# Optimization experiments

Measured on AMD Instinct MI355X. Metric: run time of the kernel, lower is better.

The kernel has to match this reference:

```python
import jax, jax.numpy as jnp
import numpy as np

N_EMBD = 2048
N_HEAD = 32
N_KV_HEADS = 8
HEAD_DIM = 64
N_REP = N_HEAD // N_KV_HEADS
MAX_SEQ_LEN = 4096
ROPE_THETA = 10000.0


def _precompute_freqs_cis(dim, end, theta=ROPE_THETA):
    freqs = 1.0 / theta ** (jnp.arange(0, dim, 2)[: dim // 2].astype(jnp.float32) / dim)
    t = jnp.arange(end, dtype=jnp.float32)
    freqs = jnp.outer(t, freqs)  # (end, dim//2)
    return jnp.cos(freqs), jnp.sin(freqs)


def setup_inputs() -> dict:
    key = jax.random.key(0)
    ks = jax.random.split(key, 5)
    B, S = 2, 2048
    x = jax.random.normal(ks[0], (B, S, N_EMBD), dtype=jnp.float32)
    # torch Linear(in, out, bias=False): y = x @ W.T, W is (out, in). We store (in, out).
    sc = 1.0 / np.sqrt(N_EMBD)
    wq = jax.random.normal(ks[1], (N_EMBD, N_EMBD), dtype=jnp.float32) * sc
    wk = jax.random.normal(ks[2], (N_EMBD, N_KV_HEADS * HEAD_DIM), dtype=jnp.float32) * sc
    wv = jax.random.normal(ks[3], (N_EMBD, N_KV_HEADS * HEAD_DIM), dtype=jnp.float32) * sc
    wo = jax.random.normal(ks[4], (N_EMBD, N_EMBD), dtype=jnp.float32) * sc
    freqs_cos, freqs_sin = _precompute_freqs_cis(HEAD_DIM, MAX_SEQ_LEN)
    return {"x": x, "wq": wq, "wk": wk, "wv": wv, "wo": wo,
            "freqs_cos": freqs_cos, "freqs_sin": freqs_sin}


def _apply_rotary(t, cos, sin):
    # t: (B, S, H, HD); interleaved real/imag pairs along last dim.
    shp = t.shape
    t2 = t.reshape(*shp[:-1], HEAD_DIM // 2, 2)
    r, i = t2[..., 0], t2[..., 1]
    out_r = r * cos - i * sin
    out_i = r * sin + i * cos
    return jnp.stack([out_r, out_i], axis=-1).reshape(shp)


def reference(x, wq, wk, wv, wo, freqs_cos, freqs_sin):
    B, S, _ = x.shape
    xq = (x @ wq).reshape(B, S, N_HEAD, HEAD_DIM)
    xk = (x @ wk).reshape(B, S, N_KV_HEADS, HEAD_DIM)
    xv = (x @ wv).reshape(B, S, N_KV_HEADS, HEAD_DIM)

    cos = freqs_cos[:S][None, :, None, :]  # (1, S, 1, HD/2)
    sin = freqs_sin[:S][None, :, None, :]
    xq = _apply_rotary(xq, cos, sin)
    xk = _apply_rotary(xk, cos, sin)

    # GQA: repeat KV heads (repeat_interleave along head dim)
    keys = jnp.repeat(xk, N_REP, axis=2)    # (B, S, H, HD)
    values = jnp.repeat(xv, N_REP, axis=2)

    scores = jnp.einsum('bqhd,bkhd->bhqk', xq, keys) / np.sqrt(HEAD_DIM)
    causal = jnp.tril(jnp.ones((S, S), dtype=bool))
    scores = jnp.where(causal, scores, -jnp.inf)
    probs = jax.nn.softmax(scores.astype(jnp.float32), axis=-1).astype(xq.dtype)
    out = jnp.einsum('bhqk,bkhd->bqhd', probs, values)  # (B, S, H, HD)
    out = out.reshape(B, S, N_EMBD)
    return out @ wo
```

## Files before the change

kernel.cpp:

```cpp
#include <hip/hip_runtime.h>
#include <hip/hip_fp16.h>
#include <stdint.h>

typedef _Float16 f16x8 __attribute__((ext_vector_type(8)));
typedef _Float16 f16x2 __attribute__((ext_vector_type(2)));
typedef float f32x4 __attribute__((ext_vector_type(4)));
typedef float f32x16 __attribute__((ext_vector_type(16)));

#define B_ 2
#define S_ 2048
#define NE 2048
#define NH 32
#define NKV 8
#define HD 64
#define NTOK (B_ * S_)
#define QKVN 3072

__device__ __forceinline__ void gld_lds16(void* lds, const void* g) {
  __builtin_amdgcn_global_load_lds(
      (const __attribute__((address_space(1))) void*)g,
      (__attribute__((address_space(3))) void*)lds, 16, 0, 0);
}

__global__ void conv_x_kernel(const float* __restrict__ x,
                              _Float16* __restrict__ xo, int n2) {
  int i = blockIdx.x * 256 + threadIdx.x;
  if (i < n2) {
    float2 v = ((const float2*)x)[i];
    f16x2 h;
    h.x = (_Float16)v.x;
    h.y = (_Float16)v.y;
    ((f16x2*)xo)[i] = h;
  }
}

__global__ void tconv_kernel(const float* __restrict__ src,
                             _Float16* __restrict__ dst,
                             int srcN, int rowoff, int ldd) {
  __shared__ float tile[32][33];
  int n0 = blockIdx.x * 32, k0 = blockIdx.y * 32;
  int tx = threadIdx.x, ty = threadIdx.y;
  for (int i = ty; i < 32; i += 8)
    tile[i][tx] = src[(size_t)(k0 + i) * srcN + n0 + tx];
  __syncthreads();
  for (int i = ty; i < 32; i += 8)
    dst[(size_t)(rowoff + n0 + i) * ldd + k0 + tx] = (_Float16)tile[tx][i];
}

template <int OUT_F32>
__global__ __launch_bounds__(256, 2) void gemm_bt(
    const _Float16* __restrict__ A, const _Float16* __restrict__ Bt,
    void* __restrict__ Cout, int M, int N, int K) {
  __shared__ _Float16 As[128 * 32];
  __shared__ _Float16 Bs[128 * 32];
  const int tid = threadIdx.x;
  const int wave = tid >> 6, lane = tid & 63;
  const int qd = lane >> 4, ln = lane & 15;
  const int m0 = blockIdx.y * 128, n0 = blockIdx.x * 128;
  const int wm = (wave >> 1) * 64, wn = (wave & 1) * 64;

  f32x4 acc[4][4] = {};

  const int srow = (lane >> 2);
  const int scol = (lane & 3) * 8;

  for (int k0 = 0; k0 < K; k0 += 32) {
    __syncthreads();
#pragma unroll
    for (int it = 0; it < 2; ++it) {
      int r = wave * 32 + it * 16 + srow;
      gld_lds16(&As[(wave * 32 + it * 16) * 32],
                A + (size_t)(m0 + r) * K + k0 + scol);
      gld_lds16(&Bs[(wave * 32 + it * 16) * 32],
                Bt + (size_t)(n0 + r) * K + k0 + scol);
    }
    __syncthreads();
    f16x8 a[4], b[4];
#pragma unroll
    for (int mt = 0; mt < 4; ++mt)
      a[mt] = *(const f16x8*)&As[(wm + mt * 16 + ln) * 32 + qd * 8];
#pragma unroll
    for (int nt = 0; nt < 4; ++nt)
      b[nt] = *(const f16x8*)&Bs[(wn + nt * 16 + ln) * 32 + qd * 8];
#pragma unroll
    for (int mt = 0; mt < 4; ++mt)
#pragma unroll
      for (int nt = 0; nt < 4; ++nt)
        acc[mt][nt] =
            __builtin_amdgcn_mfma_f32_16x16x32_f16(a[mt], b[nt], acc[mt][nt], 0, 0, 0);
  }

#pragma unroll
  for (int mt = 0; mt < 4; ++mt) {
    int row = m0 + wm + mt * 16 + qd * 4;
#pragma unroll
    for (int nt = 0; nt < 4; ++nt) {
      int col = n0 + wn + nt * 16 + ln;
#pragma unroll
      for (int r = 0; r < 4; ++r) {
        if (OUT_F32)
          ((float*)Cout)[(size_t)(row + r) * N + col] = acc[mt][nt][r];
        else
          ((_Float16*)Cout)[(size_t)(row + r) * N + col] =
              (_Float16)acc[mt][nt][r];
      }
    }
  }
}

__global__ void rope_scatter_kernel(const _Float16* __restrict__ qkv,
                                    const float* __restrict__ fcos,
                                    const float* __restrict__ fsin,
                                    _Float16* __restrict__ Qb,
                                    _Float16* __restrict__ Kb) {
  const float QSC = 0.125f * 1.44269504088896f;
  int idx = blockIdx.x * 256 + threadIdx.x;
  int t = idx / 1280;
  int col = (idx - t * 1280) * 2;
  int b = t >> 11, s = t & 2047;
  float v0 = (float)qkv[(size_t)t * QKVN + col];
  float v1 = (float)qkv[(size_t)t * QKVN + col + 1];
  _Float16* dst;
  size_t off;
  int d;
  float sc;
  if (col < 2048) {
    int h = col >> 6;
    d = col & 63;
    dst = Qb;
    off = ((size_t)(b * NH + h) * S_ + s) * HD + d;
    sc = QSC;
  } else {
    int cc = col - 2048;
    int h = cc >> 6;
    d = cc & 63;
    dst = Kb;
    off = ((size_t)(b * NKV + h) * S_ + s) * HD + d;
    sc = 1.0f;
  }
  float c = fcos[s * 32 + (d >> 1)], sn = fsin[s * 32 + (d >> 1)];
  f16x2 o;
  o.x = (_Float16)((v0 * c - v1 * sn) * sc);
  o.y = (_Float16)((v0 * sn + v1 * c) * sc);
  *(f16x2*)(dst + off) = o;
}

__global__ void vtrans_kernel(const _Float16* __restrict__ qkv,
                              _Float16* __restrict__ Vtg) {
  __shared__ _Float16 tile[64][65];
  int t0 = blockIdx.x * 64;
  int kv = blockIdx.y, b = blockIdx.z;
  int tid = threadIdx.x;
  for (int slot = tid; slot < 4096; slot += 256) {
    int r = slot >> 6, c = slot & 63;
    tile[r][c] = qkv[(size_t)(b * S_ + t0 + r) * QKVN + 2560 + kv * 64 + c];
  }
  __syncthreads();
  size_t base = ((size_t)(b * NKV + kv) * HD) * S_;
  for (int slot = tid; slot < 4096; slot += 256) {
    int d = slot >> 6, r = slot & 63;
    Vtg[base + (size_t)d * S_ + t0 + r] = tile[r][d];
  }
}

__global__ __launch_bounds__(256, 2) void attn_kernel(
    const _Float16* __restrict__ Qb, const _Float16* __restrict__ Kb,
    const _Float16* __restrict__ Vtg, _Float16* __restrict__ Ob) {
  constexpr int LDP = 72;
  constexpr float M_SHIFT = 10.0f;
  __shared__ _Float16 Ks[64 * 64];
  __shared__ _Float16 Vs[64 * 64];
  __shared__ _Float16 Ps[4 * 32 * LDP];
  const int tid = threadIdx.x;
  const int wave = tid >> 6, lane = tid & 63;
  const int mrow = lane & 31, half = lane >> 5;
  const int h = blockIdx.y, b = blockIdx.z;
  const int kvh = h >> 2;

  const _Float16* Qh = Qb + ((size_t)(b * NH + h) * S_) * HD;
  const _Float16* Kh = Kb + ((size_t)(b * NKV + kvh) * S_) * HD;
  const _Float16* Vh = Vtg + ((size_t)(b * NKV + kvh) * HD) * S_;

  const int sr = tid >> 3;
  const int scc = tid & 7;
  _Float16* Pw = &Ps[wave * 32 * LDP];

#pragma unroll
  for (int pass = 0; pass < 2; ++pass) {
    const int qt = pass ? blockIdx.x : (15 - blockIdx.x);
    const int q0 = qt * 128;
    const int nkt = 2 * qt + 2;

    const int qrow = q0 + wave * 32 + mrow;
    f16x8 aq[4];
#pragma unroll
    for (int kk = 0; kk < 4; ++kk)
      aq[kk] = *(const f16x8*)(Qh + (size_t)qrow * HD + kk * 16 + half * 8);

    f32x16 accO[2] = {};
    float lsum[16] = {};

    f16x8 kp[2], vp[2];
#pragma unroll
    for (int i = 0; i < 2; ++i) {
      kp[i] = *(const f16x8*)(Kh + (size_t)(i * 32 + sr) * HD + scc * 8);
      vp[i] = *(const f16x8*)(Vh + (size_t)(i * 32 + sr) * S_ + scc * 8);
    }
#pragma unroll
    for (int i = 0; i < 2; ++i) {
      int r = i * 32 + sr;
      *(f16x8*)&Ks[r * 64 + ((scc ^ (r & 7)) * 8)] = kp[i];
      *(f16x8*)&Vs[r * 64 + ((scc ^ (r & 7)) * 8)] = vp[i];
    }

    for (int kt = 0; kt < nkt; ++kt) {
      __syncthreads();
      if (kt + 1 < nkt) {
#pragma unroll
        for (int i = 0; i < 2; ++i) {
          kp[i] = *(const f16x8*)(Kh +
                                  (size_t)((kt + 1) * 64 + i * 32 + sr) * HD +
                                  scc * 8);
          vp[i] = *(const f16x8*)(Vh + (size_t)(i * 32 + sr) * S_ +
                                  (kt + 1) * 64 + scc * 8);
        }
      }

      f32x16 s[2];
#pragma unroll
      for (int nt = 0; nt < 2; ++nt)
#pragma unroll
        for (int r = 0; r < 16; ++r) s[nt][r] = -M_SHIFT;
#pragma unroll
      for (int kk = 0; kk < 4; ++kk) {
        int c = kk * 2 + half;
#pragma unroll
        for (int nt = 0; nt < 2; ++nt) {
          int key = nt * 32 + mrow;
          f16x8 bk = *(const f16x8*)&Ks[key * 64 + ((c ^ (key & 7)) * 8)];
          s[nt] = __builtin_amdgcn_mfma_f32_32x32x16_f16(aq[kk], bk, s[nt],
                                                         0, 0, 0);
        }
      }

      const bool edge = (kt >= nkt - 2);
#pragma unroll
      for (int nt = 0; nt < 2; ++nt)
#pragma unroll
        for (int r = 0; r < 16; ++r) {
          int rr = (r & 3) + 8 * (r >> 2) + 4 * half;
          float p = exp2f(s[nt][r]);
          if (edge) {
            int key = kt * 64 + nt * 32 + mrow;
            int qr = q0 + wave * 32 + rr;
            if (key > qr) p = 0.f;
          }
          lsum[r] += p;
          Pw[rr * LDP + nt * 32 + mrow] = (_Float16)p;
        }

      asm volatile("s_waitcnt lgkmcnt(0)" ::: "memory");
      f16x8 ap[4];
#pragma unroll
      for (int kk = 0; kk < 4; ++kk)
        ap[kk] = *(const f16x8*)&Pw[mrow * LDP + kk * 16 + half * 8];

#pragma unroll
      for (int kk = 0; kk < 4; ++kk) {
        int c = kk * 2 + half;
#pragma unroll
        for (int nt = 0; nt < 2; ++nt) {
          int d = nt * 32 + mrow;
          f16x8 bv = *(const f16x8*)&Vs[d * 64 + ((c ^ (d & 7)) * 8)];
          accO[nt] = __builtin_amdgcn_mfma_f32_32x32x16_f16(ap[kk], bv,
                                                            accO[nt], 0, 0, 0);
        }
      }

      __syncthreads();
      if (kt + 1 < nkt) {
#pragma unroll
        for (int i = 0; i < 2; ++i) {
          int r = i * 32 + sr;
          *(f16x8*)&Ks[r * 64 + ((scc ^ (r & 7)) * 8)] = kp[i];
          *(f16x8*)&Vs[r * 64 + ((scc ^ (r & 7)) * 8)] = vp[i];
        }
      }
    }

#pragma unroll
    for (int r = 0; r < 16; ++r) {
      float t = lsum[r];
#pragma unroll
      for (int off = 1; off <= 16; off <<= 1) t += __shfl_xor(t, off);
      float inv = 1.f / t;
      int rr = (r & 3) + 8 * (r >> 2) + 4 * half;
      int srow = q0 + wave * 32 + rr;
      size_t base = ((size_t)(b * S_) + srow) * NE + h * HD;
#pragma unroll
      for (int nt = 0; nt < 2; ++nt)
        Ob[base + nt * 32 + mrow] = (_Float16)(accO[nt][r] * inv);
    }
  }
}

extern "C" void kernel_launch(void* const* d_in, const int* in_sizes, int n_in,
                              void* d_out, int out_size, void* d_ws,
                              size_t ws_size, hipStream_t stream) {
  const float* x = (const float*)d_in[0];
  const float* wq = (const float*)d_in[1];
  const float* wk = (const float*)d_in[2];
  const float* wv = (const float*)d_in[3];
  const float* wo = (const float*)d_in[4];
  const float* fcos = (const float*)d_in[5];
  const float* fsin = (const float*)d_in[6];

  char* ws = (char*)d_ws;
  _Float16* xb = (_Float16*)(ws);
  _Float16* wqkv_t = (_Float16*)(ws + 16777216);
  _Float16* wo_t = (_Float16*)(ws + 29360128);
  _Float16* qkv = (_Float16*)(ws + 37748736);
  _Float16* Qb = (_Float16*)(ws + 62914560);
  _Float16* Kb = (_Float16*)(ws + 79691776);
  _Float16* Vb = (_Float16*)(ws + 83886080);
  _Float16* Ob = (_Float16*)(ws + 88080384);

  conv_x_kernel<<<16384, 256, 0, stream>>>(x, xb, (NTOK * NE) / 2);

  dim3 tb(32, 8);
  tconv_kernel<<<dim3(64, 64), tb, 0, stream>>>(wq, wqkv_t, 2048, 0, 2048);
  tconv_kernel<<<dim3(16, 64), tb, 0, stream>>>(wk, wqkv_t, 512, 2048, 2048);
  tconv_kernel<<<dim3(16, 64), tb, 0, stream>>>(wv, wqkv_t, 512, 2560, 2048);
  tconv_kernel<<<dim3(64, 64), tb, 0, stream>>>(wo, wo_t, 2048, 0, 2048);

  gemm_bt<0><<<dim3(QKVN / 128, NTOK / 128), 256, 0, stream>>>(
      xb, wqkv_t, qkv, NTOK, QKVN, NE);

  rope_scatter_kernel<<<(NTOK * 1280) / 256, 256, 0, stream>>>(qkv, fcos, fsin,
                                                               Qb, Kb);
  vtrans_kernel<<<dim3(S_ / 64, NKV, B_), 256, 0, stream>>>(qkv, Vb);

  attn_kernel<<<dim3(8, NH, B_), 256, 0, stream>>>(Qb, Kb, Vb, Ob);

  gemm_bt<1><<<dim3(NE / 128, NTOK / 128), 256, 0, stream>>>(
      Ob, wo_t, d_out, NTOK, NE, NE);
}
```

Before: 346.2 us.

## Keep attention P in registers via transposed MFMA and shrink query tile

The attention kernel swaps the MFMA operand order so scores come out transposed (keys by query). The probability tile can then be packed to fp16 and exchanged across wave halves with lane shuffles, replacing the round trip through shared memory. The query tile drops from 128 to 64 rows with 2 waves per block and twice the grid, row sums collapse to one scalar per lane, and output stores become packed 4-wide. This removes LDS traffic and a wait, at the cost of extra shuffles and less K/V reuse per block load.

```diff
diff --git a/kernel.cpp b/kernel.cpp
--- a/kernel.cpp
+++ b/kernel.cpp
@@ -3,6 +3,7 @@
 #include <stdint.h>
 
 typedef _Float16 f16x8 __attribute__((ext_vector_type(8)));
+typedef _Float16 f16x4 __attribute__((ext_vector_type(4)));
 typedef _Float16 f16x2 __attribute__((ext_vector_type(2)));
 typedef float f32x4 __attribute__((ext_vector_type(4)));
 typedef float f32x16 __attribute__((ext_vector_type(16)));
@@ -15,6 +16,10 @@
 #define HD 64
 #define NTOK (B_ * S_)
 #define QKVN 3072
+
+__device__ __forceinline__ f16x2 pk(float a, float b) {
+  return __builtin_bit_cast(f16x2, __builtin_amdgcn_cvt_pkrtz(a, b));
+}
 
 __device__ __forceinline__ void gld_lds16(void* lds, const void* g) {
   __builtin_amdgcn_global_load_lds(
@@ -163,17 +168,16 @@
   }
 }
 
-__global__ __launch_bounds__(256, 2) void attn_kernel(
+__global__ __launch_bounds__(128, 2) void attn_kernel(
     const _Float16* __restrict__ Qb, const _Float16* __restrict__ Kb,
     const _Float16* __restrict__ Vtg, _Float16* __restrict__ Ob) {
-  constexpr int LDP = 72;
   constexpr float M_SHIFT = 10.0f;
   __shared__ _Float16 Ks[64 * 64];
   __shared__ _Float16 Vs[64 * 64];
-  __shared__ _Float16 Ps[4 * 32 * LDP];
   const int tid = threadIdx.x;
   const int wave = tid >> 6, lane = tid & 63;
-  const int mrow = lane & 31, half = lane >> 5;
+  const int mrow = lane & 31;
+  const bool half = (lane >> 5) != 0;
   const int h = blockIdx.y, b = blockIdx.z;
   const int kvh = h >> 2;
 
@@ -183,45 +187,45 @@
 
   const int sr = tid >> 3;
   const int scc = tid & 7;
-  _Float16* Pw = &Ps[wave * 32 * LDP];
+  const int swz = (scc ^ (sr & 7)) * 8;
 
 #pragma unroll
   for (int pass = 0; pass < 2; ++pass) {
-    const int qt = pass ? blockIdx.x : (15 - blockIdx.x);
-    const int q0 = qt * 128;
-    const int nkt = 2 * qt + 2;
+    const int qt = pass ? blockIdx.x : (31 - blockIdx.x);
+    const int q0 = qt * 64;
+    const int nkt = qt + 1;
 
     const int qrow = q0 + wave * 32 + mrow;
     f16x8 aq[4];
 #pragma unroll
     for (int kk = 0; kk < 4; ++kk)
-      aq[kk] = *(const f16x8*)(Qh + (size_t)qrow * HD + kk * 16 + half * 8);
+      aq[kk] = *(const f16x8*)(Qh + (size_t)qrow * HD + kk * 16 +
+                               (half ? 8 : 0));
 
     f32x16 accO[2] = {};
-    float lsum[16] = {};
-
-    f16x8 kp[2], vp[2];
-#pragma unroll
-    for (int i = 0; i < 2; ++i) {
-      kp[i] = *(const f16x8*)(Kh + (size_t)(i * 32 + sr) * HD + scc * 8);
-      vp[i] = *(const f16x8*)(Vh + (size_t)(i * 32 + sr) * S_ + scc * 8);
-    }
-#pragma unroll
-    for (int i = 0; i < 2; ++i) {
-      int r = i * 32 + sr;
-      *(f16x8*)&Ks[r * 64 + ((scc ^ (r & 7)) * 8)] = kp[i];
-      *(f16x8*)&Vs[r * 64 + ((scc ^ (r & 7)) * 8)] = vp[i];
+    float lsum = 0.f;
+
+    f16x8 kp[4], vp[4];
+#pragma unroll
+    for (int i = 0; i < 4; ++i) {
+      kp[i] = *(const f16x8*)(Kh + (size_t)(sr + i * 16) * HD + scc * 8);
+      vp[i] = *(const f16x8*)(Vh + (size_t)(sr + i * 16) * S_ + scc * 8);
+    }
+#pragma unroll
+    for (int i = 0; i < 4; ++i) {
+      *(f16x8*)&Ks[(sr + i * 16) * 64 + swz] = kp[i];
+      *(f16x8*)&Vs[(sr + i * 16) * 64 + swz] = vp[i];
     }
 
     for (int kt = 0; kt < nkt; ++kt) {
       __syncthreads();
       if (kt + 1 < nkt) {
 #pragma unroll
-        for (int i = 0; i < 2; ++i) {
+        for (int i = 0; i < 4; ++i) {
           kp[i] = *(const f16x8*)(Kh +
-                                  (size_t)((kt + 1) * 64 + i * 32 + sr) * HD +
+                                  (size_t)((kt + 1) * 64 + sr + i * 16) * HD +
                                   scc * 8);
-          vp[i] = *(const f16x8*)(Vh + (size_t)(i * 32 + sr) * S_ +
+          vp[i] = *(const f16x8*)(Vh + (size_t)(sr + i * 16) * S_ +
                                   (kt + 1) * 64 + scc * 8);
         }
       }
@@ -233,74 +237,95 @@
         for (int r = 0; r < 16; ++r) s[nt][r] = -M_SHIFT;
 #pragma unroll
       for (int kk = 0; kk < 4; ++kk) {
-        int c = kk * 2 + half;
+        int c = kk * 2 + (half ? 1 : 0);
 #pragma unroll
         for (int nt = 0; nt < 2; ++nt) {
-          int key = nt * 32 + mrow;
-          f16x8 bk = *(const f16x8*)&Ks[key * 64 + ((c ^ (key & 7)) * 8)];
-          s[nt] = __builtin_amdgcn_mfma_f32_32x32x16_f16(aq[kk], bk, s[nt],
+          int krow = nt * 32 + mrow;
+          f16x8 bk = *(const f16x8*)&Ks[krow * 64 + ((c ^ (krow & 7)) * 8)];
+          s[nt] = __builtin_amdgcn_mfma_f32_32x32x16_f16(bk, aq[kk], s[nt],
                                                          0, 0, 0);
         }
       }
 
-      const bool edge = (kt >= nkt - 2);
+      const bool edge = (kt == nkt - 1);
+      float pf[2][16];
 #pragma unroll
       for (int nt = 0; nt < 2; ++nt)
 #pragma unroll
         for (int r = 0; r < 16; ++r) {
-          int rr = (r & 3) + 8 * (r >> 2) + 4 * half;
+          int key = kt * 64 + nt * 32 + (r & 3) + 8 * (r >> 2) +
+                    (half ? 4 : 0);
           float p = exp2f(s[nt][r]);
-          if (edge) {
-            int key = kt * 64 + nt * 32 + mrow;
-            int qr = q0 + wave * 32 + rr;
-            if (key > qr) p = 0.f;
-          }
-          lsum[r] += p;
-          Pw[rr * LDP + nt * 32 + mrow] = (_Float16)p;
-        }
-
-      asm volatile("s_waitcnt lgkmcnt(0)" ::: "memory");
-      f16x8 ap[4];
-#pragma unroll
-      for (int kk = 0; kk < 4; ++kk)
-        ap[kk] = *(const f16x8*)&Pw[mrow * LDP + kk * 16 + half * 8];
-
-#pragma unroll
-      for (int kk = 0; kk < 4; ++kk) {
-        int c = kk * 2 + half;
-#pragma unroll
-        for (int nt = 0; nt < 2; ++nt) {
-          int d = nt * 32 + mrow;
-          f16x8 bv = *(const f16x8*)&Vs[d * 64 + ((c ^ (d & 7)) * 8)];
-          accO[nt] = __builtin_amdgcn_mfma_f32_32x32x16_f16(ap[kk], bv,
-                                                            accO[nt], 0, 0, 0);
+          if (edge && key > qrow) p = 0.f;
+          lsum += p;
+          pf[nt][r] = p;
+        }
+
+      f16x2 P2[2][4][2];
+#pragma unroll
+      for (int nt = 0; nt < 2; ++nt)
+#pragma unroll
+        for (int c = 0; c < 4; ++c)
+#pragma unroll
+          for (int u = 0; u < 2; ++u)
+            P2[nt][c][u] = pk(pf[nt][4 * c + 2 * u], pf[nt][4 * c + 2 * u + 1]);
+
+#pragma unroll
+      for (int s4 = 0; s4 < 4; ++s4) {
+        const int ntp = s4 >> 1;
+        const int gA = (2 * s4) & 3, gB = (2 * s4 + 1) & 3;
+        f16x2 own0 = half ? P2[ntp][gB][0] : P2[ntp][gA][0];
+        f16x2 own1 = half ? P2[ntp][gB][1] : P2[ntp][gA][1];
+        f16x2 snd0 = half ? P2[ntp][gA][0] : P2[ntp][gB][0];
+        f16x2 snd1 = half ? P2[ntp][gA][1] : P2[ntp][gB][1];
+        f16x2 rcv0 = __builtin_bit_cast(
+            f16x2, __shfl_xor(__builtin_bit_cast(int, snd0), 32));
+        f16x2 rcv1 = __builtin_bit_cast(
+            f16x2, __shfl_xor(__builtin_bit_cast(int, snd1), 32));
+        union {
+          f16x2 h2[4];
+          f16x8 h8;
+        } bp;
+        bp.h2[0] = half ? rcv0 : own0;
+        bp.h2[1] = half ? rcv1 : own1;
+        bp.h2[2] = half ? own0 : rcv0;
+        bp.h2[3] = half ? own1 : rcv1;
+        const int c = 2 * s4 + (half ? 1 : 0);
+#pragma unroll
+        for (int ntd = 0; ntd < 2; ++ntd) {
+          int drow = ntd * 32 + mrow;
+          f16x8 bv = *(const f16x8*)&Vs[drow * 64 + ((c ^ (drow & 7)) * 8)];
+          accO[ntd] = __builtin_amdgcn_mfma_f32_32x32x16_f16(bv, bp.h8,
+                                                             accO[ntd], 0, 0, 0);
         }
       }
 
       __syncthreads();
       if (kt + 1 < nkt) {
 #pragma unroll
-        for (int i = 0; i < 2; ++i) {
-          int r = i * 32 + sr;
-          *(f16x8*)&Ks[r * 64 + ((scc ^ (r & 7)) * 8)] = kp[i];
-          *(f16x8*)&Vs[r * 64 + ((scc ^ (r & 7)) * 8)] = vp[i];
-        }
-      }
-    }
-
-#pragma unroll
-    for (int r = 0; r < 16; ++r) {
-      float t = lsum[r];
-#pragma unroll
-      for (int off = 1; off <= 16; off <<= 1) t += __shfl_xor(t, off);
-      float inv = 1.f / t;
-      int rr = (r & 3) + 8 * (r >> 2) + 4 * half;
-      int srow = q0 + wave * 32 + rr;
-      size_t base = ((size_t)(b * S_) + srow) * NE + h * HD;
-#pragma unroll
-      for (int nt = 0; nt < 2; ++nt)
-        Ob[base + nt * 32 + mrow] = (_Float16)(accO[nt][r] * inv);
-    }
+        for (int i = 0; i < 4; ++i) {
+          *(f16x8*)&Ks[(sr + i * 16) * 64 + swz] = kp[i];
+          *(f16x8*)&Vs[(sr + i * 16) * 64 + swz] = vp[i];
+        }
+      }
+    }
+
+    float tot = lsum + __shfl_xor(lsum, 32);
+    float inv = 1.f / tot;
+    size_t base = ((size_t)(b * S_) + qrow) * NE + h * HD;
+#pragma unroll
+    for (int ntd = 0; ntd < 2; ++ntd)
+#pragma unroll
+      for (int rq = 0; rq < 4; ++rq) {
+        int d0 = ntd * 32 + 8 * rq + (half ? 4 : 0);
+        union {
+          f16x2 h2[2];
+          f16x4 h4;
+        } o;
+        o.h2[0] = pk(accO[ntd][4 * rq + 0] * inv, accO[ntd][4 * rq + 1] * inv);
+        o.h2[1] = pk(accO[ntd][4 * rq + 2] * inv, accO[ntd][4 * rq + 3] * inv);
+        *(f16x4*)(Ob + base + d0) = o.h4;
+      }
   }
 }
 
@@ -340,7 +365,7 @@
                                                                Qb, Kb);
   vtrans_kernel<<<dim3(S_ / 64, NKV, B_), 256, 0, stream>>>(qkv, Vb);
 
-  attn_kernel<<<dim3(8, NH, B_), 256, 0, stream>>>(Qb, Kb, Vb, Ob);
+  attn_kernel<<<dim3(16, NH, B_), 128, 0, stream>>>(Qb, Kb, Vb, Ob);
 
   gemm_bt<1><<<dim3(NE / 128, NTOK / 128), 256, 0, stream>>>(
       Ob, wo_t, d_out, NTOK, NE, NE);
```

Result: faster. 327.2 us (-5.5%).
